# Optimization experiments

Hardware: AMD Instinct MI355X
Metric: run time of the kernel (lower is better)

## Reference

```python
import jax, jax.numpy as jnp
import numpy as np

DIM = 128
WH, WW = 8, 8
N = WH * WW            # tokens per window = 64
H = 8                  # num_heads
HD = DIM // H          # head_dim = 16
SCALE = HD ** -0.5
B = 2                  # true batch
NW = 1024              # windows per image (256x256 / 8x8)
B_ = B * NW            # 2048 windows total
NFT = 2                # num_frame_type
TABLE = (2 * WH - 1) * (2 * WW - 1)  # 225


def _relative_position_index():
    coords = np.stack(np.meshgrid(np.arange(WH), np.arange(WW), indexing='ij'))  # (2, WH, WW)
    cf = coords.reshape(2, -1)                        # (2, N)
    rel = cf[:, :, None] - cf[:, None, :]             # (2, N, N)
    rel = rel.transpose(1, 2, 0).astype(np.int64)     # (N, N, 2)
    rel[..., 0] += WH - 1
    rel[..., 1] += WW - 1
    rel[..., 0] *= 2 * WW - 1
    return rel.sum(-1)                                # (N, N) in [0, 224]


def setup_inputs() -> dict:
    key = jax.random.key(0)
    ks = jax.random.split(key, 12)
    x = jax.random.normal(ks[0], (B_, N, DIM), dtype=jnp.float32)
    # 0 / -100 additive window mask (shifted-window pattern surrogate)
    mask = jnp.where(jax.random.uniform(ks[1], (NW, N, N)) > 0.9, -100.0, 0.0).astype(jnp.float32)
    frame_type = jax.random.uniform(ks[2], (B, NFT), dtype=jnp.float32)
    qkv_w = jax.random.normal(ks[3], (3 * DIM, DIM), dtype=jnp.float32) * 0.02
    qkv_b = jnp.zeros((3 * DIM,), dtype=jnp.float32)
    table = jax.random.normal(ks[4], (TABLE, H), dtype=jnp.float32) * 0.02
    proj_w = jax.random.normal(ks[5], (DIM, DIM), dtype=jnp.float32) * 0.02
    proj_b = jnp.zeros((DIM,), dtype=jnp.float32)
    aff_w1 = jax.random.normal(ks[6], (16, NFT), dtype=jnp.float32) * 0.1
    aff_b1 = jnp.zeros((16,), dtype=jnp.float32)
    aff_w2 = jax.random.normal(ks[7], (2 * DIM, 16), dtype=jnp.float32) * 0.1
    rel_index = jnp.asarray(_relative_position_index(), dtype=jnp.int32)
    return {"x": x, "mask": mask, "frame_type": frame_type,
            "qkv_w": qkv_w, "qkv_b": qkv_b, "table": table,
            "proj_w": proj_w, "proj_b": proj_b,
            "aff_w1": aff_w1, "aff_b1": aff_b1, "aff_w2": aff_w2,
            "rel_index": rel_index}


def reference(x, mask, frame_type, qkv_w, qkv_b, table, proj_w, proj_b,
              aff_w1, aff_b1, aff_w2, rel_index):
    # qkv projection: (B_, N, 3C) -> (3, B_, H, N, HD)
    qkv = (x @ qkv_w.T + qkv_b).reshape(B_, N, 3, H, HD).transpose(2, 0, 3, 1, 4)
    q, k, v = qkv[0], qkv[1], qkv[2]
    attn = jnp.einsum('bhnd,bhmd->bhnm', q * SCALE, k)          # (B_, H, N, N)
    rpb = table[rel_index].transpose(2, 0, 1)                    # (H, N, N)
    attn = attn + rpb[None]
    # add window mask: (B, NW, H, N, N)
    attn = attn.reshape(B_ // NW, NW, H, N, N) + mask[None, :, None]
    attn = jax.nn.softmax(attn.reshape(B_, H, N, N), axis=-1)
    # FA affine modulation of V
    hdn = jax.nn.sigmoid(frame_type @ aff_w1.T + aff_b1)         # (B, 16)
    ap = hdn @ aff_w2.T                                          # (B, 2C)
    scale_p, bias_p = jnp.split(ap, 2, axis=-1)                  # each (B, C)
    scale_p = jnp.repeat(scale_p, B_ // B, axis=0).reshape(B_, H, 1, HD)
    bias_p = jnp.repeat(bias_p, B_ // B, axis=0).reshape(B_, H, 1, HD)
    v = jax.nn.softplus(scale_p) * v + bias_p
    out = jnp.einsum('bhnm,bhmd->bhnd', attn, v)                 # (B_, H, N, HD)
    out = out.transpose(0, 2, 1, 3).reshape(B_, N, DIM)
    return out @ proj_w.T + proj_b
```

## Files before the change

kernel.cpp:

```cpp
#include <hip/hip_runtime.h>
#include <hip/hip_bf16.h>

#define NWIN 2048
#define LOG2E 1.44269504f
#define QSCALE 0.36067376f

#define OFF_AFF 0
#define OFF_RPB 512
#define OFF_WQ  33280
#define OFF_WP  57856

typedef __attribute__((ext_vector_type(8))) __bf16 bf16x8;
typedef __attribute__((ext_vector_type(4))) float floatx4;
typedef __attribute__((ext_vector_type(4))) short short4v;

#if __has_builtin(__builtin_amdgcn_exp2f)
#define EXP2F __builtin_amdgcn_exp2f
#else
#define EXP2F exp2f
#endif

__global__ __launch_bounds__(256) void prep_kernel(
    const float* __restrict__ frame_type, const float* __restrict__ qkv_w,
    const float* __restrict__ table, const float* __restrict__ proj_w,
    const float* __restrict__ aff_w1, const float* __restrict__ aff_b1,
    const float* __restrict__ aff_w2, const int* __restrict__ rel_index,
    float* __restrict__ ws)
{
  const int gid = blockIdx.x * 256 + threadIdx.x;
  if (gid < 49152) {
    int j = gid & 7, lane = (gid >> 3) & 63, kt = (gid >> 9) & 3, nt = gid >> 11;
    int n = nt * 16 + (lane & 15);
    int k = kt * 32 + (lane >> 4) * 8 + j;
    ((__bf16*)(ws + OFF_WQ))[gid] = (__bf16)qkv_w[n * 128 + k];
  }
  if (gid < 16384) {
    int j = gid & 3, lane = (gid >> 2) & 63, nt = (gid >> 8) & 7, h = gid >> 11;
    int n = nt * 16 + (lane & 15);
    int k = h * 16 + (lane >> 4) * 4 + j;
    ((__bf16*)(ws + OFF_WP))[gid] = (__bf16)proj_w[n * 128 + k];
  }
  if (gid < 32768) {
    int h = gid >> 12, rem = gid & 4095, row = rem >> 6, col = rem & 63;
    int dst = h * 4096 + row * 64 + (col & 15) * 4 + (col >> 4);
    ws[OFF_RPB + dst] = table[rel_index[rem] * 8 + h] * LOG2E;
  }
  if (gid < 512) {
    int b = gid >> 8, c2 = gid & 255;
    float hd[16];
    #pragma unroll
    for (int j = 0; j < 16; ++j) {
      float t = frame_type[b*2+0]*aff_w1[j*2+0] + frame_type[b*2+1]*aff_w1[j*2+1] + aff_b1[j];
      hd[j] = 1.0f / (1.0f + expf(-t));
    }
    float ap = 0.f;
    #pragma unroll
    for (int j = 0; j < 16; ++j) ap += hd[j] * aff_w2[c2*16 + j];
    float r = (c2 < 128) ? ((ap > 20.f) ? ap : log1pf(expf(ap))) : ap;
    ws[OFF_AFF + gid] = r;
  }
}

__global__ __launch_bounds__(256, 3) void attn_kernel(
    const float* __restrict__ x, const float* __restrict__ mask,
    const float* __restrict__ qkv_b, const float* __restrict__ proj_b,
    const float* __restrict__ ws, float* __restrict__ out)
{
  __shared__ __attribute__((aligned(16))) __bf16 sQP[64 * 136];
  __shared__ __attribute__((aligned(16))) __bf16 sK [64 * 136];
  __shared__ __attribute__((aligned(16))) __bf16 sVT[128 * 72];

  const int w    = blockIdx.x;
  const int b    = w >> 10;
  const int tid  = threadIdx.x;
  const int wv   = tid >> 6;
  const int lane = tid & 63;
  const int quad = lane >> 4;
  const int l15  = lane & 15;
  const int row0 = wv * 16;

  bf16x8 af[4][4];
  {
    const float* xw = x + (size_t)w * 8192;
    #pragma unroll
    for (int mt = 0; mt < 4; ++mt)
      #pragma unroll
      for (int kt = 0; kt < 4; ++kt) {
        const float* p = xw + (mt*16 + l15) * 128 + kt*32 + quad*8;
        float4 f0 = *(const float4*)p;
        float4 f1 = *(const float4*)(p + 4);
        bf16x8 v;
        v[0]=(__bf16)f0.x; v[1]=(__bf16)f0.y; v[2]=(__bf16)f0.z; v[3]=(__bf16)f0.w;
        v[4]=(__bf16)f1.x; v[5]=(__bf16)f1.y; v[6]=(__bf16)f1.z; v[7]=(__bf16)f1.w;
        af[mt][kt] = v;
      }
  }

  {
    const __bf16* wq = (const __bf16*)(ws + OFF_WQ);
    for (int t = 0; t < 6; ++t) {
      const int nt = wv + t * 4;
      bf16x8 bfr[4];
      #pragma unroll
      for (int kt = 0; kt < 4; ++kt)
        bfr[kt] = *(const bf16x8*)(wq + ((size_t)(nt*4 + kt) * 64 + lane) * 8);
      const float bias = qkv_b[nt*16 + l15];
      const int col = nt*16 + l15;
      #pragma unroll
      for (int mt = 0; mt < 4; ++mt) {
        floatx4 acc = {bias, bias, bias, bias};
        #pragma unroll
        for (int kt = 0; kt < 4; ++kt)
          acc = __builtin_amdgcn_mfma_f32_16x16x32_bf16(af[mt][kt], bfr[kt], acc, 0, 0, 0);
        const int rowb = mt*16 + quad*4;
        if (nt < 8) {
          #pragma unroll
          for (int r = 0; r < 4; ++r) sQP[(rowb + r)*136 + col] = (__bf16)(acc[r] * QSCALE);
        } else if (nt < 16) {
          const int c = col - 128;
          #pragma unroll
          for (int r = 0; r < 4; ++r) sK[(rowb + r)*136 + c] = (__bf16)acc[r];
        } else {
          const int c = col - 256;
          const float sp = ws[OFF_AFF + b*256 + c];
          const float bp = ws[OFF_AFF + b*256 + 128 + c];
          #pragma unroll
          for (int r = 0; r < 4; ++r) sVT[c*72 + rowb + r] = (__bf16)fmaf(sp, acc[r], bp);
        }
      }
    }
  }
  __syncthreads();

  short4v qa[8];
  #pragma unroll
  for (int h = 0; h < 8; ++h)
    qa[h] = *(const short4v*)(&sQP[(row0 + l15)*136 + h*16 + quad*4]);

  __bf16* sP = sQP + wv * 2176;

  float mv[4][4];
  {
    const float* mrow = mask + (size_t)(w & 1023) * 4096;
    #pragma unroll
    for (int jt = 0; jt < 4; ++jt)
      #pragma unroll
      for (int r = 0; r < 4; ++r)
        mv[jt][r] = mrow[(row0 + quad*4 + r)*64 + jt*16 + l15] * LOG2E;
  }
  floatx4 pacc[8];
  #pragma unroll
  for (int nt = 0; nt < 8; ++nt) {
    float pb = proj_b[nt*16 + l15];
    pacc[nt] = (floatx4){pb, pb, pb, pb};
  }

  bf16x8 ones;
  #pragma unroll
  for (int i = 0; i < 8; ++i) ones[i] = (__bf16)1.0f;

  const float* rpb = ws + OFF_RPB;
  const __bf16* wp = (const __bf16*)(ws + OFF_WP);

  #pragma unroll 1
  for (int h = 0; h < 8; ++h) {
    floatx4 rq[4];
    #pragma unroll
    for (int r = 0; r < 4; ++r)
      rq[r] = *(const floatx4*)(rpb + h*4096 + (row0 + quad*4 + r)*64 + l15*4);
    short4v wpf[8];
    #pragma unroll
    for (int nt = 0; nt < 8; ++nt)
      wpf[nt] = *(const short4v*)(wp + ((size_t)(h*8 + nt)*64 + lane)*4);

    short4v kb[4];
    #pragma unroll
    for (int jt = 0; jt < 4; ++jt)
      kb[jt] = *(const short4v*)(&sK[(jt*16 + l15)*136 + h*16 + quad*4]);

    floatx4 s[4];
    #pragma unroll
    for (int jt = 0; jt < 4; ++jt) {
      floatx4 ci;
      #pragma unroll
      for (int r = 0; r < 4; ++r) ci[r] = rq[r][jt] + mv[jt][r];
      s[jt] = __builtin_amdgcn_mfma_f32_16x16x16bf16_1k(qa[h], kb[jt], ci, 0, 0, 0);
    }
    #pragma unroll
    for (int jt = 0; jt < 4; ++jt)
      #pragma unroll
      for (int r = 0; r < 4; ++r)
        sP[(quad*4 + r)*72 + jt*16 + l15] = (__bf16)EXP2F(s[jt][r]);

    floatx4 o2 = {0.f,0.f,0.f,0.f}, s2 = {0.f,0.f,0.f,0.f};
    #pragma unroll
    for (int kt = 0; kt < 2; ++kt) {
      bf16x8 pa = *(const bf16x8*)(&sP[l15*72 + kt*32 + quad*8]);
      bf16x8 vb = *(const bf16x8*)(&sVT[(h*16 + l15)*72 + kt*32 + quad*8]);
      o2 = __builtin_amdgcn_mfma_f32_16x16x32_bf16(vb, pa, o2, 0, 0, 0);
      s2 = __builtin_amdgcn_mfma_f32_16x16x32_bf16(ones, pa, s2, 0, 0, 0);
    }
    const float inv = 1.0f / s2[0];
    union { short4v s; __bf16 hh[4]; } u;
    #pragma unroll
    for (int r = 0; r < 4; ++r) u.hh[r] = (__bf16)(o2[r] * inv);
    #pragma unroll
    for (int nt = 0; nt < 8; ++nt)
      pacc[nt] = __builtin_amdgcn_mfma_f32_16x16x16bf16_1k(u.s, wpf[nt], pacc[nt], 0, 0, 0);
  }

  {
    float* ow = out + (size_t)w * 8192;
    #pragma unroll
    for (int nt = 0; nt < 8; ++nt)
      #pragma unroll
      for (int r = 0; r < 4; ++r)
        ow[(row0 + quad*4 + r)*128 + nt*16 + l15] = pacc[nt][r];
  }
}

extern "C" void kernel_launch(void* const* d_in, const int* in_sizes, int n_in,
                              void* d_out, int out_size, void* d_ws, size_t ws_size,
                              hipStream_t stream)
{
  const float* x          = (const float*)d_in[0];
  const float* mask       = (const float*)d_in[1];
  const float* frame_type = (const float*)d_in[2];
  const float* qkv_w      = (const float*)d_in[3];
  const float* qkv_b      = (const float*)d_in[4];
  const float* table      = (const float*)d_in[5];
  const float* proj_w     = (const float*)d_in[6];
  const float* proj_b     = (const float*)d_in[7];
  const float* aff_w1     = (const float*)d_in[8];
  const float* aff_b1     = (const float*)d_in[9];
  const float* aff_w2     = (const float*)d_in[10];
  const int*   rel_index  = (const int*)d_in[11];
  float* ws   = (float*)d_ws;
  float* outp = (float*)d_out;

  prep_kernel<<<192, 256, 0, stream>>>(frame_type, qkv_w, table, proj_w,
                                       aff_w1, aff_b1, aff_w2, rel_index, ws);
  attn_kernel<<<NWIN, 256, 0, stream>>>(x, mask, qkv_b, proj_b, ws, outp);
}
```

Baseline: 218.4 us.

## Keep Q and P in registers via transposed MFMA and permuted key order

Q is now computed per wave straight into registers with a transposed MFMA, and the shared Q/P buffer is removed. K rows are stored in a permuted order so the transposed score tile's accumulator layout feeds the PV MFMA directly as the B operand, with no LDS round trip for P. The rpb and mask loads are remapped to match. The head loop is fully unrolled and occupancy is raised to 4 blocks. This cuts LDS traffic and footprint, at the cost of higher register pressure under the tighter launch bound.

```diff
diff --git a/kernel.cpp b/kernel.cpp
--- a/kernel.cpp
+++ b/kernel.cpp
@@ -41,9 +41,8 @@
     ((__bf16*)(ws + OFF_WP))[gid] = (__bf16)proj_w[n * 128 + k];
   }
   if (gid < 32768) {
-    int h = gid >> 12, rem = gid & 4095, row = rem >> 6, col = rem & 63;
-    int dst = h * 4096 + row * 64 + (col & 15) * 4 + (col >> 4);
-    ws[OFF_RPB + dst] = table[rel_index[rem] * 8 + h] * LOG2E;
+    int h = gid >> 12, rem = gid & 4095;
+    ws[OFF_RPB + gid] = table[rel_index[rem] * 8 + h] * LOG2E;
   }
   if (gid < 512) {
     int b = gid >> 8, c2 = gid & 255;
@@ -61,12 +60,11 @@
   }
 }
 
-__global__ __launch_bounds__(256, 3) void attn_kernel(
+__global__ __launch_bounds__(256, 4) void attn_kernel(
     const float* __restrict__ x, const float* __restrict__ mask,
     const float* __restrict__ qkv_b, const float* __restrict__ proj_b,
     const float* __restrict__ ws, float* __restrict__ out)
 {
-  __shared__ __attribute__((aligned(16))) __bf16 sQP[64 * 136];
   __shared__ __attribute__((aligned(16))) __bf16 sK [64 * 136];
   __shared__ __attribute__((aligned(16))) __bf16 sVT[128 * 72];
 
@@ -96,10 +94,12 @@
       }
   }
 
-  {
-    const __bf16* wq = (const __bf16*)(ws + OFF_WQ);
-    for (int t = 0; t < 6; ++t) {
-      const int nt = wv + t * 4;
+  const __bf16* wq = (const __bf16*)(ws + OFF_WQ);
+
+  {
+    #pragma unroll
+    for (int t = 0; t < 4; ++t) {
+      const int nt = 8 + ((t >> 1) << 3) + ((t & 1) << 2) + wv;
       bf16x8 bfr[4];
       #pragma unroll
       for (int kt = 0; kt < 4; ++kt)
@@ -112,42 +112,66 @@
         #pragma unroll
         for (int kt = 0; kt < 4; ++kt)
           acc = __builtin_amdgcn_mfma_f32_16x16x32_bf16(af[mt][kt], bfr[kt], acc, 0, 0, 0);
-        const int rowb = mt*16 + quad*4;
-        if (nt < 8) {
+        if (nt < 16) {
+          const int c = col - 128;
+          const int srow0 = ((((quad & 1) << 1) + (mt >> 1)) << 4)
+                          + ((((mt & 1) << 1) | (quad >> 1)) << 2);
           #pragma unroll
-          for (int r = 0; r < 4; ++r) sQP[(rowb + r)*136 + col] = (__bf16)(acc[r] * QSCALE);
-        } else if (nt < 16) {
-          const int c = col - 128;
-          #pragma unroll
-          for (int r = 0; r < 4; ++r) sK[(rowb + r)*136 + c] = (__bf16)acc[r];
+          for (int r = 0; r < 4; ++r) sK[(srow0 + r)*136 + c] = (__bf16)acc[r];
         } else {
           const int c = col - 256;
           const float sp = ws[OFF_AFF + b*256 + c];
           const float bp = ws[OFF_AFF + b*256 + 128 + c];
+          const int rowb = mt*16 + quad*4;
           #pragma unroll
           for (int r = 0; r < 4; ++r) sVT[c*72 + rowb + r] = (__bf16)fmaf(sp, acc[r], bp);
         }
       }
     }
   }
+
+  bf16x8 aq[4];
+  #pragma unroll
+  for (int kt = 0; kt < 4; ++kt) aq[kt] = af[0][kt];
+  #pragma unroll
+  for (int mt = 1; mt < 4; ++mt)
+    if (wv == mt) {
+      #pragma unroll
+      for (int kt = 0; kt < 4; ++kt) aq[kt] = af[mt][kt];
+    }
+
+  short4v qa[8];
+  {
+    #pragma unroll
+    for (int nt = 0; nt < 8; ++nt) {
+      bf16x8 bfr[4];
+      #pragma unroll
+      for (int kt = 0; kt < 4; ++kt)
+        bfr[kt] = *(const bf16x8*)(wq + ((size_t)(nt*4 + kt) * 64 + lane) * 8);
+      floatx4 acc = *(const floatx4*)(qkv_b + nt*16 + quad*4);
+      #pragma unroll
+      for (int kt = 0; kt < 4; ++kt)
+        acc = __builtin_amdgcn_mfma_f32_16x16x32_bf16(bfr[kt], aq[kt], acc, 0, 0, 0);
+      union { short4v s; __bf16 h4[4]; } u;
+      #pragma unroll
+      for (int r = 0; r < 4; ++r) u.h4[r] = (__bf16)(acc[r] * QSCALE);
+      qa[nt] = u.s;
+    }
+  }
   __syncthreads();
 
-  short4v qa[8];
-  #pragma unroll
-  for (int h = 0; h < 8; ++h)
-    qa[h] = *(const short4v*)(&sQP[(row0 + l15)*136 + h*16 + quad*4]);
-
-  __bf16* sP = sQP + wv * 2176;
-
-  float mv[4][4];
-  {
-    const float* mrow = mask + (size_t)(w & 1023) * 4096;
-    #pragma unroll
-    for (int jt = 0; jt < 4; ++jt)
-      #pragma unroll
-      for (int r = 0; r < 4; ++r)
-        mv[jt][r] = mrow[(row0 + quad*4 + r)*64 + jt*16 + l15] * LOG2E;
-  }
+  floatx4 mv[4];
+  {
+    const float* mrow = mask + (size_t)(w & 1023) * 4096 + (row0 + l15) * 64;
+    #pragma unroll
+    for (int jt = 0; jt < 4; ++jt) {
+      const int joff = ((jt & 1) << 5) + ((jt >> 1) << 2) + (quad << 3);
+      floatx4 m4 = *(const floatx4*)(mrow + joff);
+      #pragma unroll
+      for (int r = 0; r < 4; ++r) mv[jt][r] = m4[r] * LOG2E;
+    }
+  }
+
   floatx4 pacc[8];
   #pragma unroll
   for (int nt = 0; nt < 8; ++nt) {
@@ -162,48 +186,52 @@
   const float* rpb = ws + OFF_RPB;
   const __bf16* wp = (const __bf16*)(ws + OFF_WP);
 
-  #pragma unroll 1
+  #pragma unroll
   for (int h = 0; h < 8; ++h) {
     floatx4 rq[4];
     #pragma unroll
-    for (int r = 0; r < 4; ++r)
-      rq[r] = *(const floatx4*)(rpb + h*4096 + (row0 + quad*4 + r)*64 + l15*4);
+    for (int jt = 0; jt < 4; ++jt) {
+      const int joff = ((jt & 1) << 5) + ((jt >> 1) << 2) + (quad << 3);
+      rq[jt] = *(const floatx4*)(rpb + h*4096 + (row0 + l15)*64 + joff);
+    }
+    short4v kb[4];
+    #pragma unroll
+    for (int jt = 0; jt < 4; ++jt)
+      kb[jt] = *(const short4v*)(&sK[(jt*16 + l15)*136 + h*16 + quad*4]);
+
+    floatx4 s[4];
+    #pragma unroll
+    for (int jt = 0; jt < 4; ++jt) {
+      floatx4 ci = rq[jt] + mv[jt];
+      s[jt] = __builtin_amdgcn_mfma_f32_16x16x16bf16_1k(kb[jt], qa[h], ci, 0, 0, 0);
+    }
+
+    union { bf16x8 v; __bf16 e[8]; } p0, p1;
+    #pragma unroll
+    for (int r = 0; r < 4; ++r) {
+      p0.e[r]     = (__bf16)EXP2F(s[0][r]);
+      p0.e[4 + r] = (__bf16)EXP2F(s[2][r]);
+      p1.e[r]     = (__bf16)EXP2F(s[1][r]);
+      p1.e[4 + r] = (__bf16)EXP2F(s[3][r]);
+    }
+
+    bf16x8 vb0 = *(const bf16x8*)(&sVT[(h*16 + l15)*72 + quad*8]);
+    bf16x8 vb1 = *(const bf16x8*)(&sVT[(h*16 + l15)*72 + 32 + quad*8]);
+    floatx4 o2 = {0.f,0.f,0.f,0.f}, sm = {0.f,0.f,0.f,0.f};
+    o2 = __builtin_amdgcn_mfma_f32_16x16x32_bf16(vb0, p0.v, o2, 0, 0, 0);
+    sm = __builtin_amdgcn_mfma_f32_16x16x32_bf16(ones, p0.v, sm, 0, 0, 0);
+    o2 = __builtin_amdgcn_mfma_f32_16x16x32_bf16(vb1, p1.v, o2, 0, 0, 0);
+    sm = __builtin_amdgcn_mfma_f32_16x16x32_bf16(ones, p1.v, sm, 0, 0, 0);
+
+    const float inv = 1.0f / sm[0];
+    union { short4v s; __bf16 hh[4]; } u;
+    #pragma unroll
+    for (int r = 0; r < 4; ++r) u.hh[r] = (__bf16)(o2[r] * inv);
+
     short4v wpf[8];
     #pragma unroll
     for (int nt = 0; nt < 8; ++nt)
       wpf[nt] = *(const short4v*)(wp + ((size_t)(h*8 + nt)*64 + lane)*4);
-
-    short4v kb[4];
-    #pragma unroll
-    for (int jt = 0; jt < 4; ++jt)
-      kb[jt] = *(const short4v*)(&sK[(jt*16 + l15)*136 + h*16 + quad*4]);
-
-    floatx4 s[4];
-    #pragma unroll
-    for (int jt = 0; jt < 4; ++jt) {
-      floatx4 ci;
-      #pragma unroll
-      for (int r = 0; r < 4; ++r) ci[r] = rq[r][jt] + mv[jt][r];
-      s[jt] = __builtin_amdgcn_mfma_f32_16x16x16bf16_1k(qa[h], kb[jt], ci, 0, 0, 0);
-    }
-    #pragma unroll
-    for (int jt = 0; jt < 4; ++jt)
-      #pragma unroll
-      for (int r = 0; r < 4; ++r)
-        sP[(quad*4 + r)*72 + jt*16 + l15] = (__bf16)EXP2F(s[jt][r]);
-
-    floatx4 o2 = {0.f,0.f,0.f,0.f}, s2 = {0.f,0.f,0.f,0.f};
-    #pragma unroll
-    for (int kt = 0; kt < 2; ++kt) {
-      bf16x8 pa = *(const bf16x8*)(&sP[l15*72 + kt*32 + quad*8]);
-      bf16x8 vb = *(const bf16x8*)(&sVT[(h*16 + l15)*72 + kt*32 + quad*8]);
-      o2 = __builtin_amdgcn_mfma_f32_16x16x32_bf16(vb, pa, o2, 0, 0, 0);
-      s2 = __builtin_amdgcn_mfma_f32_16x16x32_bf16(ones, pa, s2, 0, 0, 0);
-    }
-    const float inv = 1.0f / s2[0];
-    union { short4v s; __bf16 hh[4]; } u;
-    #pragma unroll
-    for (int r = 0; r < 4; ++r) u.hh[r] = (__bf16)(o2[r] * inv);
     #pragma unroll
     for (int nt = 0; nt < 8; ++nt)
       pacc[nt] = __builtin_amdgcn_mfma_f32_16x16x16bf16_1k(u.s, wpf[nt], pacc[nt], 0, 0, 0);
```

After: 248.0 us. +13.6%, slower.
